# Kernel optimization log

Measured on AMD Instinct MI355X. Metric: run time of the kernel, lower is better.

The kernel has to match this reference:

```python
import jax, jax.numpy as jnp
import numpy as np

LN_EPS = 1e-5

def layer_norm(x, w, b):
    mu = jnp.mean(x, axis=-1, keepdims=True)
    var = jnp.mean(jnp.square(x - mu), axis=-1, keepdims=True)
    return (x - mu) * jax.lax.rsqrt(var + LN_EPS) * w + b

def adaptive_mask_np(aa, bb, ada_para=0.2):
    # True = disallowed (matches torch ~bool mask). Static shapes -> numpy.
    adaptive_num = int(bb * ada_para)
    cc = bb // aa
    i = np.arange(aa)
    start = i * cc
    end = start + cc + adaptive_num
    over = end > bb - 1
    start = np.where(over, np.maximum(start - (end - (bb - 1)), 0), start)
    end = np.where(over, bb, end)
    cols = np.arange(bb)
    allowed = (cols[None, :] >= start[:, None]) & (cols[None, :] < end[:, None])
    return jnp.asarray(~allowed)  # [aa, bb] bool

def setup_inputs() -> dict:
    key = jax.random.key(0)
    ks = jax.random.split(key, 20)
    Lq, Lk, B, d, dff = 512, 4096, 4, 512, 2048
    s = lambda k, shape: jax.random.normal(k, shape, dtype=jnp.float32) * 0.02
    inp = {
        'tgt': jax.random.normal(ks[0], (Lq, B, d), dtype=jnp.float32),
        'memory': jax.random.normal(ks[1], (Lk, B, d), dtype=jnp.float32),
        'Wq': s(ks[2], (d, d)), 'bq': jnp.zeros((d,), jnp.float32),
        'Wk': s(ks[3], (d, d)), 'bk': jnp.zeros((d,), jnp.float32),
        'Wv': s(ks[4], (d, d)), 'bv': jnp.zeros((d,), jnp.float32),
        'Wo': s(ks[5], (d, d)), 'bo': jnp.zeros((d,), jnp.float32),
        'W1': s(ks[6], (dff, d)), 'b1': jnp.zeros((dff,), jnp.float32),
        'W2': s(ks[7], (d, dff)), 'b2': jnp.zeros((d,), jnp.float32),
        'ln1_w': jnp.ones((d,), jnp.float32), 'ln1_b': jnp.zeros((d,), jnp.float32),
        'ln2_w': jnp.ones((d,), jnp.float32), 'ln2_b': jnp.zeros((d,), jnp.float32),
        'ln3_w': jnp.ones((d,), jnp.float32), 'ln3_b': jnp.zeros((d,), jnp.float32),
        'ln4_w': jnp.ones((d,), jnp.float32), 'ln4_b': jnp.zeros((d,), jnp.float32),
    }
    return inp

def reference(tgt, memory, Wq, bq, Wk, bk, Wv, bv, Wo, bo, W1, b1, W2, b2,
              ln1_w, ln1_b, ln2_w, ln2_b, ln3_w, ln3_b, ln4_w, ln4_b):
    Lq, B, d = tgt.shape
    Lk = memory.shape[0]
    H = 8
    hd = d // H
    scale = 1.0 / jnp.sqrt(jnp.asarray(hd, tgt.dtype))

    t = layer_norm(tgt, ln1_w, ln1_b)      # [Lq,B,d]
    m = layer_norm(memory, ln2_w, ln2_b)   # [Lk,B,d]

    mask = adaptive_mask_np(Lq, Lk, 0.2)   # [Lq,Lk] bool, True=masked

    q = (t @ Wq.T + bq).reshape(Lq, B, H, hd)
    k = (m @ Wk.T + bk).reshape(Lk, B, H, hd)
    v = (m @ Wv.T + bv).reshape(Lk, B, H, hd)

    scores = jnp.einsum('qbhd,kbhd->bhqk', q * scale, k)
    scores = jnp.where(mask[None, None], -jnp.inf, scores)
    p = jax.nn.softmax(scores, axis=-1)                   # [B,H,Lq,Lk]
    attn_weights = jnp.mean(p, axis=1)                    # [B,Lq,Lk] (avg over heads)

    ctx = jnp.einsum('bhqk,kbhd->qbhd', p, v).reshape(Lq, B, d)
    tgt2 = ctx @ Wo.T + bo

    x = t + tgt2                       # dropout1 = identity (eval)
    x = layer_norm(x, ln3_w, ln3_b)
    ff = jax.nn.relu(x @ W1.T + b1) @ W2.T + b2
    x = x + ff                         # dropout2 = identity (eval)
    x = layer_norm(x, ln4_w, ln4_b)
    return (x, attn_weights)
```

## Files before the change

kernel.cpp:

```cpp
#include <hip/hip_runtime.h>
#include <hip/hip_bf16.h>

typedef __hip_bfloat16 bf16_t;
typedef __bf16 bf16x8 __attribute__((ext_vector_type(8)));
typedef float f32x4 __attribute__((ext_vector_type(4)));

#define LQ 512
#define LK 4096
#define BATCH 4
#define DMODEL 512
#define NHEAD 8
#define HEADDIM 64
#define DFF 2048
#define LN_EPS 1e-5f

#define KSTR 2080
#define VSTR 4128

__device__ inline float tofl(float x) { return x; }
__device__ inline float tofl(bf16_t x) { return __bfloat162float(x); }
__device__ inline void stfl(float* p, float v) { *p = v; }
__device__ inline void stfl(bf16_t* p, float v) { *p = __float2bfloat16(v); }

__device__ __forceinline__ void gld_lds16(const bf16_t* g, void* lds_base) {
    __builtin_amdgcn_global_load_lds(
        (const __attribute__((address_space(1))) uint32_t*)g,
        (__attribute__((address_space(3))) uint32_t*)lds_base, 16, 0, 0);
}

__global__ void prep_kernel(const float* __restrict__ s0, const float* __restrict__ s1,
                            const float* __restrict__ s2, const float* __restrict__ s3,
                            const float* __restrict__ s4,
                            bf16_t* __restrict__ wqkvo, bf16_t* __restrict__ w1bf) {
    int t = blockIdx.x * 256 + threadIdx.x;
    int which = t >> 16;
    int idx = (t & 65535) * 4;
    const float* s; bf16_t* d;
    if (which < 4) {
        s = (which == 0 ? s0 : which == 1 ? s1 : which == 2 ? s2 : s3);
        d = wqkvo + (size_t)which * 262144;
    } else {
        s = s4 + (size_t)(which - 4) * 262144;
        d = w1bf + (size_t)(which - 4) * 262144;
    }
    float4 v = *(const float4*)(s + idx);
    d[idx + 0] = __float2bfloat16(v.x);
    d[idx + 1] = __float2bfloat16(v.y);
    d[idx + 2] = __float2bfloat16(v.z);
    d[idx + 3] = __float2bfloat16(v.w);
}

__global__ void conv_w2(const float* __restrict__ s, bf16_t* __restrict__ d) {
    int i = (blockIdx.x * 256 + threadIdx.x) * 4;
    float4 v = *(const float4*)(s + i);
    d[i + 0] = __float2bfloat16(v.x);
    d[i + 1] = __float2bfloat16(v.y);
    d[i + 2] = __float2bfloat16(v.z);
    d[i + 3] = __float2bfloat16(v.w);
}

template <typename TOUT, bool DUAL>
__global__ void ln_kernel(const float* __restrict__ in, const float* __restrict__ w,
                          const float* __restrict__ b, TOUT* __restrict__ out1,
                          float* __restrict__ out2) {
    __shared__ float red[256];
    const int row = blockIdx.x;
    const int tid = threadIdx.x;
    const float* x = in + (size_t)row * DMODEL;
    float v0 = x[tid];
    float v1 = x[tid + 256];

    red[tid] = v0 + v1;
    __syncthreads();
    for (int s = 128; s > 0; s >>= 1) { if (tid < s) red[tid] += red[tid + s]; __syncthreads(); }
    float mu = red[0] * (1.0f / DMODEL);
    __syncthreads();

    float d0 = v0 - mu, d1 = v1 - mu;
    red[tid] = d0 * d0 + d1 * d1;
    __syncthreads();
    for (int s = 128; s > 0; s >>= 1) { if (tid < s) red[tid] += red[tid + s]; __syncthreads(); }
    float inv = rsqrtf(red[0] * (1.0f / DMODEL) + LN_EPS);

    float r0 = d0 * inv * w[tid] + b[tid];
    float r1 = d1 * inv * w[tid + 256] + b[tid + 256];
    TOUT* o = out1 + (size_t)row * DMODEL;
    stfl(&o[tid], r0);
    stfl(&o[tid + 256], r1);
    if (DUAL) {
        float* o2 = out2 + (size_t)row * DMODEL;
        o2[tid] = r0;
        o2[tid + 256] = r1;
    }
}

__global__ void ln12_kernel(const float* __restrict__ tgt, const float* __restrict__ memory,
                            const float* __restrict__ w1, const float* __restrict__ b1,
                            const float* __restrict__ w2, const float* __restrict__ b2,
                            bf16_t* __restrict__ t_bf, float* __restrict__ t_f32,
                            bf16_t* __restrict__ m_buf) {
    __shared__ float red[256];
    const int row = blockIdx.x;
    const int tid = threadIdx.x;
    const float* in; const float* w; const float* b;
    bf16_t* o1; float* o2; bool dual;
    if (row < 2048) {
        in = tgt + (size_t)row * DMODEL; w = w1; b = b1;
        o1 = t_bf + (size_t)row * DMODEL; o2 = t_f32 + (size_t)row * DMODEL; dual = true;
    } else {
        int r2 = row - 2048;
        in = memory + (size_t)r2 * DMODEL; w = w2; b = b2;
        o1 = m_buf + (size_t)r2 * DMODEL; o2 = nullptr; dual = false;
    }
    float v0 = in[tid];
    float v1 = in[tid + 256];
    red[tid] = v0 + v1;
    __syncthreads();
    for (int s = 128; s > 0; s >>= 1) { if (tid < s) red[tid] += red[tid + s]; __syncthreads(); }
    float mu = red[0] * (1.0f / DMODEL);
    __syncthreads();
    float d0 = v0 - mu, d1 = v1 - mu;
    red[tid] = d0 * d0 + d1 * d1;
    __syncthreads();
    for (int s = 128; s > 0; s >>= 1) { if (tid < s) red[tid] += red[tid + s]; __syncthreads(); }
    float inv = rsqrtf(red[0] * (1.0f / DMODEL) + LN_EPS);
    float r0 = d0 * inv * w[tid] + b[tid];
    float r1 = d1 * inv * w[tid + 256] + b[tid + 256];
    o1[tid] = __float2bfloat16(r0);
    o1[tid + 256] = __float2bfloat16(r1);
    if (dual) {
        o2[tid] = r0;
        o2[tid + 256] = r1;
    }
}

template <int TN, typename TC, bool RELU, bool RESID, bool KREMAP = false>
__global__ __launch_bounds__(256) void gemm_mfma(
        const bf16_t* __restrict__ A, const bf16_t* __restrict__ B,
        const float* __restrict__ bias, const float* __restrict__ resid,
        TC* __restrict__ C, int M, int N, int K) {
    __shared__ uint4 As4[1024];
    __shared__ uint4 Bs4[TN * 8];

    const int tid = threadIdx.x;
    const int lane = tid & 63;
    const int wave = tid >> 6;
    const int row16 = lane & 15;
    const int quad = lane >> 4;
    const int n0 = blockIdx.x * TN;
    const int m0 = blockIdx.y * 128;

    constexpr int MI = (TN == 128) ? 4 : 2;
    const int wy = (TN == 128) ? (wave >> 1) : wave;
    const int wx = (TN == 128) ? (wave & 1) : 0;
    const int m_base = wy * ((TN == 128) ? 64 : 32);
    const int n_base = wx * 64;

    const int rr = lane >> 3;
    const int kc = (lane & 7) ^ rr;
    const int kx = row16 & 7;

    const bf16_t* AsE = (const bf16_t*)As4;
    const bf16_t* BsE = (const bf16_t*)Bs4;

    f32x4 acc[MI][4] = {};

    for (int k0 = 0; k0 < K; k0 += 64) {
#pragma unroll
        for (int it = 0; it < 4; it++) {
            int issue = it * 4 + wave;
            int r = issue * 8 + rr;
            gld_lds16(A + (size_t)(m0 + r) * K + k0 + kc * 8, &As4[issue * 64]);
        }
#pragma unroll
        for (int it = 0; it < TN / 32; it++) {
            int issue = it * 4 + wave;
            int r = issue * 8 + rr;
            gld_lds16(B + (size_t)(n0 + r) * K + k0 + kc * 8, &Bs4[issue * 64]);
        }
        __syncthreads();
#pragma unroll
        for (int s = 0; s < 2; s++) {
            const int kq = s * 4 + quad;
            const int kcs = (kq ^ kx) * 8;
            bf16x8 af[MI], bfr[4];
#pragma unroll
            for (int i = 0; i < MI; i++)
                af[i] = *(const bf16x8*)&AsE[(m_base + i * 16 + row16) * 64 + kcs];
#pragma unroll
            for (int j = 0; j < 4; j++)
                bfr[j] = *(const bf16x8*)&BsE[(n_base + j * 16 + row16) * 64 + kcs];
#pragma unroll
            for (int i = 0; i < MI; i++)
#pragma unroll
                for (int j = 0; j < 4; j++)
                    acc[i][j] = __builtin_amdgcn_mfma_f32_16x16x32_bf16(af[i], bfr[j], acc[i][j], 0, 0, 0);
        }
        __syncthreads();
    }

#pragma unroll
    for (int i = 0; i < MI; i++) {
#pragma unroll
        for (int j = 0; j < 4; j++) {
            int col = n0 + n_base + j * 16 + row16;
            float bsv = bias[col];
#pragma unroll
            for (int r = 0; r < 4; r++) {
                int row = m0 + m_base + i * 16 + quad * 4 + r;
                float val = acc[i][j][r] + bsv;
                if (RESID) val += resid[(size_t)row * N + col];
                if (RELU) val = fmaxf(val, 0.0f);
                size_t caddr = KREMAP
                    ? ((size_t)(row >> 2) * KSTR + (size_t)(row & 3) * 512 + col)
                    : ((size_t)row * N + col);
                stfl(&C[caddr], val);
            }
        }
    }
}

__global__ __launch_bounds__(256) void transpose_kv(const bf16_t* __restrict__ kb,
                                                    bf16_t* __restrict__ kT) {
    __shared__ bf16_t tile[64][80];
    const int kt = blockIdx.x * 64;
    const int ct = blockIdx.y * 64;
    const int b  = blockIdx.z;
    const int t = threadIdx.x;
    {
        int kl = t >> 2, cl = (t & 3) * 16;
        const bf16_t* src = kb + ((size_t)(kt + kl) * 4 + b) * 512 + ct + cl;
        *(uint4*)&tile[kl][cl]     = *(const uint4*)src;
        *(uint4*)&tile[kl][cl + 8] = *(const uint4*)(src + 8);
    }
    __syncthreads();
    {
        int cl2 = t >> 2, ks = (t & 3) * 16;
        __attribute__((aligned(16))) bf16_t vals[16];
#pragma unroll
        for (int j = 0; j < 16; j++) vals[j] = tile[ks + j][cl2];
        bf16_t* dst = kT + ((size_t)b * 512 + ct + cl2) * VSTR + kt + ks;
        *(uint4*)dst       = *(const uint4*)&vals[0];
        *(uint4*)(dst + 8) = *(const uint4*)&vals[8];
    }
}

__global__ __launch_bounds__(512, 1) void attn_mfma(
        const bf16_t* __restrict__ qb,
        const bf16_t* __restrict__ kb,
        const bf16_t* __restrict__ vT,
        bf16_t* __restrict__ ctx,
        float* __restrict__ attn_out) {
    extern __shared__ char smem[];
    bf16_t* Ps   = (bf16_t*)smem;
    bf16_t* Qs   = (bf16_t*)(smem + 115712);
    bf16_t* Zrow = (bf16_t*)(smem + 115712 + 8320);
    float*  Ls   = (float*)(smem + 115712 + 8320 + 1808);

    const int blk = blockIdx.x;
    const int b  = (blk & 7) >> 1;
    const int qt = ((blk >> 3) << 1) | (blk & 1);
    const int q0 = qt * 8;
    const int tid = threadIdx.x;
    const int lane = tid & 63;
    const int h = tid >> 6;
    const int hoffg = h * HEADDIM;
    const int row16 = lane & 15;
    const int quad = lane >> 4;

    int us; { int s = q0 * 8, e = s + 827; if (e > 4095) s = 3268; us = s; }
    int sq[4], eq[4];
#pragma unroll
    for (int r = 0; r < 4; r++) {
        int ql = quad * 4 + r;
        if (ql < 8) {
            int s = (q0 + ql) * 8, e = s + 827;
            if (e > 4095) { s = 3268; e = 4096; }
            sq[r] = s; eq[r] = e;
        } else { sq[r] = 0; eq[r] = 0; }
    }

    {
        int r = tid >> 6, coff = (tid & 63) * 8;
        *(uint4*)&Qs[r * 520 + coff] =
            *(const uint4*)(qb + ((size_t)(q0 + r) * 4 + b) * 512 + coff);
        if (tid < 113) { uint4 z = {0, 0, 0, 0}; *(uint4*)&Zrow[tid * 8] = z; }
    }
    __syncthreads();

    const bf16_t* q0p = (row16 < 8) ? &Qs[row16 * 520 + hoffg + quad * 8] : &Zrow[0];
    const bf16_t* q1p = (row16 < 8) ? &Qs[row16 * 520 + hoffg + 32 + quad * 8] : &Zrow[8];
    const bf16x8 aq0 = *(const bf16x8*)q0p;
    const bf16x8 aq1 = *(const bf16x8*)q1p;

    float l[4] = {0.f, 0.f, 0.f, 0.f};
#pragma unroll 4
    for (int it = 0; it < 56; ++it) {
        int key = us + it * 16 + row16;
        int key_eff = key > 4095 ? 4095 : key;
        const bf16_t* kr = kb + (size_t)key_eff * KSTR + b * 512 + hoffg;
        bf16x8 bk0 = *(const bf16x8*)(kr + quad * 8);
        bf16x8 bk1 = *(const bf16x8*)(kr + 32 + quad * 8);
        f32x4 acc = {};
        acc = __builtin_amdgcn_mfma_f32_16x16x32_bf16(aq0, bk0, acc, 0, 0, 0);
        acc = __builtin_amdgcn_mfma_f32_16x16x32_bf16(aq1, bk1, acc, 0, 0, 0);
#pragma unroll
        for (int r = 0; r < 4; r++) {
            int ql = quad * 4 + r;
            bool valid = (key >= sq[r]) && (key < eq[r]);
            float p = valid ? __expf(0.125f * acc[r]) : 0.0f;
            l[r] += p;
            if (ql < 8) Ps[(h * 8 + ql) * 904 + it * 16 + row16] = __float2bfloat16(p);
        }
    }
#pragma unroll
    for (int off = 1; off < 16; off <<= 1) {
#pragma unroll
        for (int r = 0; r < 4; r++) l[r] += __shfl_xor(l[r], off, 64);
    }
    float linv[4];
#pragma unroll
    for (int r = 0; r < 4; r++) linv[r] = 1.0f / l[r];
    if (row16 == 0) {
#pragma unroll
        for (int r = 0; r < 4; r++) {
            int ql = quad * 4 + r;
            if (ql < 8) Ls[h * 8 + ql] = linv[r];
        }
    }
    __syncthreads();

    f32x4 o[4] = {};
#pragma unroll 2
    for (int it = 0; it < 28; ++it) {
        const bf16_t* ap_src = (row16 < 8) ? &Ps[(h * 8 + row16) * 904 + it * 32 + quad * 8]
                                           : &Zrow[0];
        bf16x8 ap = *(const bf16x8*)ap_src;
#pragma unroll
        for (int nt = 0; nt < 4; ++nt) {
            const bf16_t* vr = vT + ((size_t)(b * 512 + hoffg + nt * 16 + row16)) * VSTR
                               + us + it * 32 + quad * 8;
            bf16x8 bv = *(const bf16x8*)vr;
            o[nt] = __builtin_amdgcn_mfma_f32_16x16x32_bf16(ap, bv, o[nt], 0, 0, 0);
        }
    }

    {
        int qq = h;
        float ls[8];
#pragma unroll
        for (int hh = 0; hh < 8; ++hh) ls[hh] = 0.125f * Ls[hh * 8 + qq];
        float* rowp = attn_out + ((size_t)b * LQ + q0 + qq) * LK;
        const bf16_t* ps = Ps + qq * 904;
        for (int it = 0; it < 16; ++it) {
            int c4 = (it * 64 + lane) * 4;
            float4 v = {0.f, 0.f, 0.f, 0.f};
            int off = c4 - us;
            if (off >= -3 && off < 896) {
#pragma unroll
                for (int e = 0; e < 4; ++e) {
                    int pc = off + e;
                    float s = 0.f;
                    if (pc >= 0 && pc < 896) {
#pragma unroll
                        for (int hh = 0; hh < 8; ++hh)
                            s += ls[hh] * tofl(ps[hh * 8 * 904 + pc]);
                    }
                    (&v.x)[e] = s;
                }
            }
            *(float4*)(rowp + c4) = v;
        }
    }

#pragma unroll
    for (int nt = 0; nt < 4; nt++) {
#pragma unroll
        for (int r = 0; r < 4; r++) {
            int ql = quad * 4 + r;
            if (ql < 8) {
                ctx[((size_t)(q0 + ql) * 4 + b) * 512 + hoffg + nt * 16 + row16] =
                    __float2bfloat16(o[nt][r] * linv[r]);
            }
        }
    }
}

extern "C" void kernel_launch(void* const* d_in, const int* in_sizes, int n_in,
                              void* d_out, int out_size, void* d_ws, size_t ws_size,
                              hipStream_t stream) {
    const float* tgt    = (const float*)d_in[0];
    const float* memory = (const float*)d_in[1];
    const float* Wq = (const float*)d_in[2];
    const float* bq = (const float*)d_in[3];
    const float* Wk = (const float*)d_in[4];
    const float* bk = (const float*)d_in[5];
    const float* Wv = (const float*)d_in[6];
    const float* bv = (const float*)d_in[7];
    const float* Wo = (const float*)d_in[8];
    const float* bo = (const float*)d_in[9];
    const float* W1 = (const float*)d_in[10];
    const float* b1 = (const float*)d_in[11];
    const float* W2 = (const float*)d_in[12];
    const float* b2 = (const float*)d_in[13];
    const float* ln1w = (const float*)d_in[14];
    const float* ln1b = (const float*)d_in[15];
    const float* ln2w = (const float*)d_in[16];
    const float* ln2b = (const float*)d_in[17];
    const float* ln3w = (const float*)d_in[18];
    const float* ln3b = (const float*)d_in[19];
    const float* ln4w = (const float*)d_in[20];
    const float* ln4b = (const float*)d_in[21];

    const size_t M1 = (size_t)LQ * BATCH;
    const size_t M2 = (size_t)LK * BATCH;
    const size_t SZ1 = M1 * DMODEL;

    char* wsb = (char*)d_ws;
    const size_t MB = 1 << 20;
    bf16_t* m_buf   = (bf16_t*)(wsb + 0 * MB);
    bf16_t* vT_buf  = (bf16_t*)(wsb + 0 * MB);
    bf16_t* h_buf   = (bf16_t*)(wsb + 0 * MB);
    bf16_t* k_buf   = (bf16_t*)(wsb + 17 * MB);
    float*  xres    = (float*)(wsb + 17 * MB);
    float*  xln_f   = (float*)(wsb + 21 * MB);
    float*  x2_buf  = (float*)(wsb + 25 * MB);
    bf16_t* W2_bf   = (bf16_t*)(wsb + 34 * MB);
    bf16_t* v_buf   = (bf16_t*)(wsb + 34 * MB);
    bf16_t* t_bf    = (bf16_t*)(wsb + 50 * MB);
    bf16_t* xln_bf  = (bf16_t*)(wsb + 50 * MB);
    float*  t_f32   = (float*)(wsb + 52 * MB);
    bf16_t* q_bf    = (bf16_t*)(wsb + 56 * MB);
    bf16_t* ctx_buf = (bf16_t*)(wsb + 58 * MB);
    bf16_t* wqkvo   = (bf16_t*)(wsb + 60 * MB);
    bf16_t* W1_bf   = (bf16_t*)(wsb + 62 * MB);

    bf16_t* Wq_bf = wqkvo;
    bf16_t* Wk_bf = wqkvo + 262144;
    bf16_t* Wv_bf = wqkvo + 2 * 262144;
    bf16_t* Wo_bf = wqkvo + 3 * 262144;

    float* out_x    = (float*)d_out;
    float* out_attn = out_x + SZ1;

    prep_kernel<<<dim3(2048), dim3(256), 0, stream>>>(
        Wq, Wk, Wv, Wo, W1, wqkvo, W1_bf);

    ln12_kernel<<<dim3(M1 + M2), dim3(256), 0, stream>>>(
        tgt, memory, ln1w, ln1b, ln2w, ln2b, t_bf, t_f32, m_buf);

    gemm_mfma<64, bf16_t, false, false><<<dim3(8, 16), dim3(256), 0, stream>>>(
        t_bf, Wq_bf, bq, nullptr, q_bf, M1, DMODEL, DMODEL);
    gemm_mfma<128, bf16_t, false, false, true><<<dim3(4, 128), dim3(256), 0, stream>>>(
        m_buf, Wk_bf, bk, nullptr, k_buf, M2, DMODEL, DMODEL);
    gemm_mfma<128, bf16_t, false, false><<<dim3(4, 128), dim3(256), 0, stream>>>(
        m_buf, Wv_bf, bv, nullptr, v_buf, M2, DMODEL, DMODEL);

    transpose_kv<<<dim3(64, 8, 4), dim3(256), 0, stream>>>(v_buf, vT_buf);

    conv_w2<<<dim3(1024), dim3(256), 0, stream>>>(W2, W2_bf);

    const int attn_lds = 115712 + 8320 + 1808 + 256;
    hipFuncSetAttribute((const void*)attn_mfma,
                        hipFuncAttributeMaxDynamicSharedMemorySize, attn_lds);
    attn_mfma<<<dim3(256), dim3(512), attn_lds, stream>>>(
        q_bf, k_buf, vT_buf, ctx_buf, out_attn);

    gemm_mfma<64, float, false, true><<<dim3(8, 16), dim3(256), 0, stream>>>(
        ctx_buf, Wo_bf, bo, t_f32, xres, M1, DMODEL, DMODEL);

    ln_kernel<bf16_t, true><<<dim3(M1), dim3(256), 0, stream>>>(xres, ln3w, ln3b, xln_bf, xln_f);

    gemm_mfma<128, bf16_t, true, false><<<dim3(16, 16), dim3(256), 0, stream>>>(
        xln_bf, W1_bf, b1, nullptr, h_buf, M1, DFF, DMODEL);

    gemm_mfma<64, float, false, true><<<dim3(8, 16), dim3(256), 0, stream>>>(
        h_buf, W2_bf, b2, xln_f, x2_buf, M1, DMODEL, DFF);

    ln_kernel<float, false><<<dim3(M1), dim3(256), 0, stream>>>(x2_buf, ln4w, ln4b, out_x, nullptr);
}
```

Baseline: 317.6 us.

## Double-buffer K and V register prefetch in attention QK and PV loops

The QK and PV loops are restructured into groups of 8 and 4 iterations. Global loads for the next group are issued into a second register buffer while MFMAs consume the current one, so memory latency overlaps with compute. The first V group is prefetched during the last QK group. The block-wide barrier between QK and PV is moved after PV, since each wave reads only its own head's P rows. This costs many extra VGPRs for the buffers and risks spills or lower occupancy.

```diff
diff --git a/kernel.cpp b/kernel.cpp
--- a/kernel.cpp
+++ b/kernel.cpp
@@ -245,6 +245,65 @@
     }
 }
 
+__device__ __forceinline__ void qk_issue(const bf16_t* kb_base, int us, int g,
+                                         int row16, bf16x8 (&b0)[8], bf16x8 (&b1)[8]) {
+#pragma unroll
+    for (int j = 0; j < 8; ++j) {
+        int key = us + (g * 8 + j) * 16 + row16;
+        int key_eff = key > 4095 ? 4095 : key;
+        const bf16_t* kr = kb_base + (size_t)key_eff * KSTR;
+        b0[j] = *(const bf16x8*)kr;
+        b1[j] = *(const bf16x8*)(kr + 32);
+    }
+}
+
+__device__ __forceinline__ void qk_compute(int g, bf16x8 (&b0)[8], bf16x8 (&b1)[8],
+        const bf16x8 aq0, const bf16x8 aq1, float (&l)[4], bf16_t* PsH,
+        int row16, int quad, const int (&sq)[4], const int (&eq)[4], int us) {
+#pragma unroll
+    for (int j = 0; j < 8; ++j) {
+        int it = g * 8 + j;
+        f32x4 acc = {};
+        acc = __builtin_amdgcn_mfma_f32_16x16x32_bf16(aq0, b0[j], acc, 0, 0, 0);
+        acc = __builtin_amdgcn_mfma_f32_16x16x32_bf16(aq1, b1[j], acc, 0, 0, 0);
+        int key = us + it * 16 + row16;
+#pragma unroll
+        for (int r = 0; r < 4; r++) {
+            int ql = quad * 4 + r;
+            bool valid = (key >= sq[r]) && (key < eq[r]);
+            float p = valid ? __expf(0.125f * acc[r]) : 0.0f;
+            l[r] += p;
+            if (ql < 8) PsH[ql * 904 + it * 16 + row16] = __float2bfloat16(p);
+        }
+    }
+}
+
+__device__ __forceinline__ void pv_issue(const bf16_t* vbase, int g, int row16, int quad,
+                                         bf16x8 (&vb)[4][4]) {
+#pragma unroll
+    for (int j = 0; j < 4; ++j) {
+        int it = g * 4 + j;
+#pragma unroll
+        for (int nt = 0; nt < 4; ++nt)
+            vb[j][nt] = *(const bf16x8*)(vbase + (size_t)(nt * 16 + row16) * VSTR
+                                         + it * 32 + quad * 8);
+    }
+}
+
+__device__ __forceinline__ void pv_compute(int g, bf16x8 (&vb)[4][4], const bf16_t* PsH,
+        const bf16_t* Zrow, int row16, int quad, f32x4 (&o)[4]) {
+#pragma unroll
+    for (int j = 0; j < 4; ++j) {
+        int it = g * 4 + j;
+        const bf16_t* ap_src = (row16 < 8) ? &PsH[row16 * 904 + it * 32 + quad * 8]
+                                           : &Zrow[0];
+        bf16x8 ap = *(const bf16x8*)ap_src;
+#pragma unroll
+        for (int nt = 0; nt < 4; ++nt)
+            o[nt] = __builtin_amdgcn_mfma_f32_16x16x32_bf16(ap, vb[j][nt], o[nt], 0, 0, 0);
+    }
+}
+
 __global__ __launch_bounds__(512, 1) void attn_mfma(
         const bf16_t* __restrict__ qb,
         const bf16_t* __restrict__ kb,
@@ -293,26 +352,23 @@
     const bf16x8 aq0 = *(const bf16x8*)q0p;
     const bf16x8 aq1 = *(const bf16x8*)q1p;
 
+    bf16_t* PsH = Ps + h * 8 * 904;
+    const bf16_t* kb_base = kb + b * 512 + hoffg + quad * 8;
+
+    bf16x8 ka0[8], ka1[8], kc0[8], kc1[8];
     float l[4] = {0.f, 0.f, 0.f, 0.f};
-#pragma unroll 4
-    for (int it = 0; it < 56; ++it) {
-        int key = us + it * 16 + row16;
-        int key_eff = key > 4095 ? 4095 : key;
-        const bf16_t* kr = kb + (size_t)key_eff * KSTR + b * 512 + hoffg;
-        bf16x8 bk0 = *(const bf16x8*)(kr + quad * 8);
-        bf16x8 bk1 = *(const bf16x8*)(kr + 32 + quad * 8);
-        f32x4 acc = {};
-        acc = __builtin_amdgcn_mfma_f32_16x16x32_bf16(aq0, bk0, acc, 0, 0, 0);
-        acc = __builtin_amdgcn_mfma_f32_16x16x32_bf16(aq1, bk1, acc, 0, 0, 0);
-#pragma unroll
-        for (int r = 0; r < 4; r++) {
-            int ql = quad * 4 + r;
-            bool valid = (key >= sq[r]) && (key < eq[r]);
-            float p = valid ? __expf(0.125f * acc[r]) : 0.0f;
-            l[r] += p;
-            if (ql < 8) Ps[(h * 8 + ql) * 904 + it * 16 + row16] = __float2bfloat16(p);
-        }
-    }
+    qk_issue(kb_base, us, 0, row16, ka0, ka1);
+    for (int gg = 0; gg < 3; ++gg) {
+        qk_issue(kb_base, us, 2 * gg + 1, row16, kc0, kc1);
+        qk_compute(2 * gg, ka0, ka1, aq0, aq1, l, PsH, row16, quad, sq, eq, us);
+        qk_issue(kb_base, us, 2 * gg + 2, row16, ka0, ka1);
+        qk_compute(2 * gg + 1, kc0, kc1, aq0, aq1, l, PsH, row16, quad, sq, eq, us);
+    }
+    bf16x8 va[4][4], vb_[4][4];
+    const bf16_t* vbase = vT + (size_t)(b * 512 + hoffg) * VSTR + us;
+    pv_issue(vbase, 0, row16, quad, va);
+    qk_compute(6, ka0, ka1, aq0, aq1, l, PsH, row16, quad, sq, eq, us);
+
 #pragma unroll
     for (int off = 1; off < 16; off <<= 1) {
 #pragma unroll
@@ -328,22 +384,17 @@
             if (ql < 8) Ls[h * 8 + ql] = linv[r];
         }
     }
-    __syncthreads();
 
     f32x4 o[4] = {};
-#pragma unroll 2
-    for (int it = 0; it < 28; ++it) {
-        const bf16_t* ap_src = (row16 < 8) ? &Ps[(h * 8 + row16) * 904 + it * 32 + quad * 8]
-                                           : &Zrow[0];
-        bf16x8 ap = *(const bf16x8*)ap_src;
-#pragma unroll
-        for (int nt = 0; nt < 4; ++nt) {
-            const bf16_t* vr = vT + ((size_t)(b * 512 + hoffg + nt * 16 + row16)) * VSTR
-                               + us + it * 32 + quad * 8;
-            bf16x8 bv = *(const bf16x8*)vr;
-            o[nt] = __builtin_amdgcn_mfma_f32_16x16x32_bf16(ap, bv, o[nt], 0, 0, 0);
-        }
-    }
+    for (int gg = 0; gg < 3; ++gg) {
+        pv_issue(vbase, 2 * gg + 1, row16, quad, vb_);
+        pv_compute(2 * gg, va, PsH, Zrow, row16, quad, o);
+        pv_issue(vbase, 2 * gg + 2, row16, quad, va);
+        pv_compute(2 * gg + 1, vb_, PsH, Zrow, row16, quad, o);
+    }
+    pv_compute(6, va, PsH, Zrow, row16, quad, o);
+
+    __syncthreads();
 
     {
         int qq = h;
```

After: 305.8 us. 1.04x faster.
